# Optimization experiments

Measured on AMD Instinct MI355X. Metric: run time of the kernel, lower is better.

## Reference

```python
import jax, jax.numpy as jnp
import numpy as np

N = 30000        # nodes
E = 480000       # edges (before self-loops)
F_IN = 512       # input feature dim
HID = 64         # per-head hidden dim
HEADS = 4
WIDTH = HID * HEADS  # 256, concat heads
LAYERS = 3
NCLS = 40
NEG_SLOPE = 0.2


def setup_inputs() -> dict:
    key = jax.random.key(0)
    ks = jax.random.split(key, 16)
    def p(k, shape, scale=0.1):
        return jax.random.normal(k, shape, dtype=jnp.float32) * scale
    return {
        "x": jax.random.normal(ks[0], (N, F_IN), dtype=jnp.float32),
        "edge_index": jax.random.randint(ks[1], (2, E), 0, N, dtype=jnp.int32),
        # layer 1: F_IN -> HEADS*HID (concat)
        "W1": p(ks[2], (F_IN, WIDTH)), "as1": p(ks[3], (HEADS, HID)), "ad1": p(ks[4], (HEADS, HID)), "b1": p(ks[5], (WIDTH,)),
        # layer 2: WIDTH -> WIDTH
        "W2": p(ks[6], (WIDTH, WIDTH)), "as2": p(ks[7], (HEADS, HID)), "ad2": p(ks[8], (HEADS, HID)), "b2": p(ks[9], (WIDTH,)),
        # layer 3: WIDTH -> WIDTH
        "W3": p(ks[10], (WIDTH, WIDTH)), "as3": p(ks[11], (HEADS, HID)), "ad3": p(ks[12], (HEADS, HID)), "b3": p(ks[13], (WIDTH,)),
        # JK='cat' output head: WIDTH*LAYERS -> NCLS
        "Wo": p(ks[14], (WIDTH * LAYERS, NCLS)), "bo": p(ks[15], (NCLS,)),
    }


def gat_layer(x, Wm, a_src, a_dst, b, src, dst):
    # PyG GATConv (concat=True, eval mode): h = xW reshaped [N,H,C];
    # e_ij = leaky_relu(a_src.h_j + a_dst.h_i) for edge j->i, softmax over dst groups.
    n = x.shape[0]
    H, C = a_src.shape
    h = (x @ Wm).reshape(n, H, C)                      # [N,H,C]
    es = jnp.sum(h * a_src, axis=-1)                   # [N,H]
    ed = jnp.sum(h * a_dst, axis=-1)                   # [N,H]
    e = jax.nn.leaky_relu(es[src] + ed[dst], NEG_SLOPE)  # [Etot,H]
    m = jax.ops.segment_max(e, dst, num_segments=n)    # stable softmax per dst node
    w = jnp.exp(e - m[dst])
    den = jax.ops.segment_sum(w, dst, num_segments=n)
    alpha = w / den[dst]                               # [Etot,H]
    out = jax.ops.segment_sum(h[src] * alpha[:, :, None], dst, num_segments=n)  # [N,H,C]
    return out.reshape(n, H * C) + b


def reference(x, edge_index, W1, as1, ad1, b1, W2, as2, ad2, b2, W3, as3, ad3, b3, Wo, bo):
    # add self-loops (PyG GATConv default)
    loops = jnp.arange(N, dtype=edge_index.dtype)
    src = jnp.concatenate([edge_index[0], loops])
    dst = jnp.concatenate([edge_index[1], loops])
    # dropout is identity in eval mode
    h1 = jax.nn.relu(gat_layer(x, W1, as1, ad1, b1, src, dst))
    h2 = jax.nn.relu(gat_layer(h1, W2, as2, ad2, b2, src, dst))
    h3 = jax.nn.relu(gat_layer(h2, W3, as3, ad3, b3, src, dst))
    h = jnp.concatenate([h1, h2, h3], axis=-1)         # JK 'cat': [N, WIDTH*LAYERS]
    return h @ Wo + bo                                 # [N, NCLS]
```

## Files before the change

kernel.cpp:

```cpp
#include <hip/hip_runtime.h>

#define N_NODES 30000
#define N_EDGES 480000
#define ETOT    510000
#define F_IN    512
#define WIDTH   256
#define NCLS    40
#define KCAT    768
#define NPAD    48

typedef __attribute__((ext_vector_type(8))) short short8;
typedef __attribute__((ext_vector_type(4))) float f32x4;

__device__ __forceinline__ unsigned short f2bf(float f){
  unsigned u = __float_as_uint(f);
  u += 0x7fffu + ((u >> 16) & 1u);
  return (unsigned short)(u >> 16);
}
__device__ __forceinline__ float b2f(unsigned short s){
  return __uint_as_float(((unsigned)s) << 16);
}

__global__ void transpose_w_kernel(const float* __restrict__ W, unsigned short* __restrict__ Wt,
                                   int K, int Nc){
  int k = blockIdx.x * blockDim.x + threadIdx.x;
  int n = blockIdx.y;
  if (k < K) Wt[(size_t)n * K + k] = f2bf(W[(size_t)k * Nc + n]);
}

__global__ void transpose_wo_kernel(const float* __restrict__ Wo, unsigned short* __restrict__ WoT){
  int i = blockIdx.x * blockDim.x + threadIdx.x;
  if (i < NPAD * KCAT){
    int c = i / KCAT, k = i - c * KCAT;
    WoT[i] = (c < NCLS) ? f2bf(Wo[(size_t)k * NCLS + c]) : (unsigned short)0;
  }
}

__global__ void zero_kernel(int* __restrict__ p, int n){
  int i = blockIdx.x * blockDim.x + threadIdx.x;
  if (i < n) p[i] = 0;
}

__global__ void hist_kernel(const int* __restrict__ ei, int* __restrict__ counts){
  int e = blockIdx.x * blockDim.x + threadIdx.x;
  if (e < ETOT){
    int d = (e < N_EDGES) ? ei[N_EDGES + e] : (e - N_EDGES);
    atomicAdd(&counts[d], 1);
  }
}

__global__ __launch_bounds__(1024) void scan_kernel(const int* __restrict__ counts,
                                                    int* __restrict__ offsets,
                                                    int* __restrict__ cursor, int n){
  __shared__ int wsum[16];
  int tid = threadIdx.x, lane = tid & 63, wid = tid >> 6;
  int running = 0;
  int nchunks = (n + 1023) >> 10;
  for (int ch = 0; ch < nchunks; ++ch){
    int i = (ch << 10) + tid;
    int v = (i < n) ? counts[i] : 0;
    int x = v;
    #pragma unroll
    for (int off = 1; off < 64; off <<= 1){
      int t = __shfl_up(x, off, 64);
      if (lane >= off) x += t;
    }
    if (lane == 63) wsum[wid] = x;
    __syncthreads();
    if (wid == 0){
      int s = (lane < 16) ? wsum[lane] : 0;
      #pragma unroll
      for (int off = 1; off < 16; off <<= 1){
        int t = __shfl_up(s, off, 64);
        if (lane >= off) s += t;
      }
      if (lane < 16) wsum[lane] = s;
    }
    __syncthreads();
    int waveprefix = (wid > 0) ? wsum[wid - 1] : 0;
    int excl = x - v + waveprefix + running;
    if (i < n){ offsets[i] = excl; cursor[i] = excl; }
    running += wsum[15];
    __syncthreads();
  }
  if (tid == 0) offsets[n] = running;
}

__global__ void scatter_kernel(const int* __restrict__ ei, int* __restrict__ cursor,
                               int* __restrict__ srcs){
  int e = blockIdx.x * blockDim.x + threadIdx.x;
  if (e < ETOT){
    int s, d;
    if (e < N_EDGES){ s = ei[e]; d = ei[N_EDGES + e]; }
    else { s = e - N_EDGES; d = s; }
    int pos = atomicAdd(&cursor[d], 1);
    srcs[pos] = s;
  }
}

#define BM 64
#define BK 32

template<bool AF32>
__global__ __launch_bounds__(256) void gemm_fused_kernel(const void* __restrict__ Araw,
                                                         const unsigned short* __restrict__ Bt,
                                                         const float* __restrict__ a_s,
                                                         const float* __restrict__ a_d,
                                                         float* __restrict__ es,
                                                         float* __restrict__ ed,
                                                         unsigned short* __restrict__ hb,
                                                         int M, int K){
  __shared__ unsigned short Als[4 * 64 * 8];
  __shared__ unsigned short Bls[4 * 256 * 8];
  int tid = threadIdx.x;
  int lane = tid & 63, wid = tid >> 6;
  int l15 = lane & 15, quad = lane >> 4;
  int m0 = blockIdx.x * BM;

  f32x4 acc[4][4];
  #pragma unroll
  for (int rt = 0; rt < 4; ++rt)
    #pragma unroll
    for (int ct = 0; ct < 4; ++ct) acc[rt][ct] = (f32x4){0.f, 0.f, 0.f, 0.f};

  int ar = tid & 63, ac = tid >> 6;
  int agrow = m0 + ar; if (agrow >= M) agrow = M - 1;

  for (int k0 = 0; k0 < K; k0 += BK){
    __syncthreads();
    if (AF32){
      const float* Af = (const float*)Araw + (size_t)agrow * K + k0 + 8 * ac;
      float4 v0 = *(const float4*)(Af);
      float4 v1 = *(const float4*)(Af + 4);
      ushort4 p0 = {f2bf(v0.x), f2bf(v0.y), f2bf(v0.z), f2bf(v0.w)};
      ushort4 p1 = {f2bf(v1.x), f2bf(v1.y), f2bf(v1.z), f2bf(v1.w)};
      *(ushort4*)(&Als[(ac * 64 + ar) * 8])     = p0;
      *(ushort4*)(&Als[(ac * 64 + ar) * 8 + 4]) = p1;
    } else {
      const unsigned short* Ab = (const unsigned short*)Araw;
      uint4 av = *(const uint4*)(Ab + (size_t)agrow * K + k0 + 8 * ac);
      *(uint4*)(&Als[(ac * 64 + ar) * 8]) = av;
    }
    {
      const unsigned short* src = Bt + (size_t)tid * K + k0;
      uint4 b0 = *(const uint4*)(src);
      uint4 b1 = *(const uint4*)(src + 8);
      uint4 b2 = *(const uint4*)(src + 16);
      uint4 b3 = *(const uint4*)(src + 24);
      *(uint4*)(&Bls[(0 * 256 + tid) * 8]) = b0;
      *(uint4*)(&Bls[(1 * 256 + tid) * 8]) = b1;
      *(uint4*)(&Bls[(2 * 256 + tid) * 8]) = b2;
      *(uint4*)(&Bls[(3 * 256 + tid) * 8]) = b3;
    }
    __syncthreads();
    short8 af[4], bf[4];
    #pragma unroll
    for (int rt = 0; rt < 4; ++rt)
      af[rt] = *(const short8*)(&Als[(quad * 64 + rt * 16 + l15) * 8]);
    #pragma unroll
    for (int ct = 0; ct < 4; ++ct)
      bf[ct] = *(const short8*)(&Bls[(quad * 256 + wid * 64 + ct * 16 + l15) * 8]);
    #pragma unroll
    for (int rt = 0; rt < 4; ++rt)
      #pragma unroll
      for (int ct = 0; ct < 4; ++ct)
        acc[rt][ct] = __builtin_amdgcn_mfma_f32_16x16x32_bf16(af[rt], bf[ct], acc[rt][ct], 0, 0, 0);
  }

  int colbase = wid * 64;

  #pragma unroll
  for (int rt = 0; rt < 4; ++rt){
    int row0 = m0 + rt * 16 + quad * 4;
    #pragma unroll
    for (int i = 0; i < 4; ++i){
      int grow = row0 + i;
      unsigned vo[4];
      #pragma unroll
      for (int ct = 0; ct < 4; ++ct){
        unsigned lo = (unsigned)f2bf(acc[rt][ct][i]);
        unsigned hi = (unsigned)__shfl_xor((int)lo, 1, 64);
        vo[ct] = lo | (hi << 16);
      }
      if ((l15 & 1) == 0 && grow < M){
        unsigned short* hrow = hb + (size_t)grow * WIDTH + colbase + l15;
        *(unsigned*)(hrow)      = vo[0];
        *(unsigned*)(hrow + 16) = vo[1];
        *(unsigned*)(hrow + 32) = vo[2];
        *(unsigned*)(hrow + 48) = vo[3];
      }
    }
  }

  float asv[4], adv[4];
  #pragma unroll
  for (int ct = 0; ct < 4; ++ct){
    asv[ct] = a_s[wid * 64 + ct * 16 + l15];
    adv[ct] = a_d[wid * 64 + ct * 16 + l15];
  }
  #pragma unroll
  for (int rt = 0; rt < 4; ++rt){
    int row0 = m0 + rt * 16 + quad * 4;
    #pragma unroll
    for (int i = 0; i < 4; ++i){
      float se = acc[rt][0][i] * asv[0] + acc[rt][1][i] * asv[1]
               + acc[rt][2][i] * asv[2] + acc[rt][3][i] * asv[3];
      float sd = acc[rt][0][i] * adv[0] + acc[rt][1][i] * adv[1]
               + acc[rt][2][i] * adv[2] + acc[rt][3][i] * adv[3];
      #pragma unroll
      for (int off = 1; off < 16; off <<= 1){
        se += __shfl_xor(se, off, 64);
        sd += __shfl_xor(sd, off, 64);
      }
      int grow = row0 + i;
      if (l15 == 0 && grow < M){
        es[grow * 4 + wid] = se;
        ed[grow * 4 + wid] = sd;
      }
    }
  }
}

__global__ __launch_bounds__(256) void agg_kernel(const int* __restrict__ offsets,
                                                  const int* __restrict__ srcs,
                                                  const float* __restrict__ es,
                                                  const float* __restrict__ ed,
                                                  const unsigned short* __restrict__ hb,
                                                  const float* __restrict__ bias,
                                                  unsigned short* __restrict__ hout){
  __shared__ float eLds[8][64][4];
  __shared__ int   sLds[8][64];
  int wid = threadIdx.x >> 6;
  int lane = threadIdx.x & 63;
  int half = lane >> 5, l32 = lane & 31;
  int slot = wid * 2 + half;
  int n = blockIdx.x * 8 + slot;
  int base = offsets[n];
  int deg = offsets[n + 1] - base;
  float4 edv = *(const float4*)(ed + n * 4);

  float m0 = -1e30f, m1 = -1e30f, m2 = -1e30f, m3 = -1e30f;
  for (int i = l32; i < deg; i += 32){
    int s = srcs[base + i];
    float4 ev = *(const float4*)(es + s * 4);
    float e0 = ev.x + edv.x, e1 = ev.y + edv.y, e2 = ev.z + edv.z, e3 = ev.w + edv.w;
    e0 = e0 > 0.f ? e0 : 0.2f * e0;
    e1 = e1 > 0.f ? e1 : 0.2f * e1;
    e2 = e2 > 0.f ? e2 : 0.2f * e2;
    e3 = e3 > 0.f ? e3 : 0.2f * e3;
    if (i < 64){
      sLds[slot][i] = s;
      *(float4*)(&eLds[slot][i][0]) = (float4){e0, e1, e2, e3};
    }
    m0 = fmaxf(m0, e0); m1 = fmaxf(m1, e1); m2 = fmaxf(m2, e2); m3 = fmaxf(m3, e3);
  }
  #pragma unroll
  for (int off = 1; off < 32; off <<= 1){
    m0 = fmaxf(m0, __shfl_xor(m0, off, 64));
    m1 = fmaxf(m1, __shfl_xor(m1, off, 64));
    m2 = fmaxf(m2, __shfl_xor(m2, off, 64));
    m3 = fmaxf(m3, __shfl_xor(m3, off, 64));
  }
  int head = l32 >> 3;
  float mh  = (head == 0) ? m0 : (head == 1) ? m1 : (head == 2) ? m2 : m3;
  float edh = (head == 0) ? edv.x : (head == 1) ? edv.y : (head == 2) ? edv.z : edv.w;

  float2 a0 = {0.f,0.f}, a1 = {0.f,0.f}, a2 = {0.f,0.f}, a3 = {0.f,0.f};
  float den = 0.f;
  const unsigned short* hcol = hb + 8 * l32;
  for (int i = 0; i < deg; i += 8){
    int sidx[8]; float w[8];
    #pragma unroll
    for (int u = 0; u < 8; ++u){
      int idx = i + u;
      bool v = idx < deg;
      float le; int s;
      if (idx < 64 || !v){
        int ic = v ? idx : 0;
        if (ic >= 64) ic = 0;
        s  = sLds[slot][ic];
        le = eLds[slot][ic][head];
      } else {
        s = srcs[base + idx];
        float e = es[s * 4 + head] + edh;
        le = e > 0.f ? e : 0.2f * e;
      }
      sidx[u] = s;
      w[u] = v ? __expf(le - mh) : 0.f;
    }
    uint4 hv[8];
    #pragma unroll
    for (int u = 0; u < 8; ++u)
      hv[u] = *(const uint4*)(hcol + (size_t)sidx[u] * WIDTH);
    #pragma unroll
    for (int u = 0; u < 8; ++u){
      float wu = w[u];
      den += wu;
      a0.x += wu * __uint_as_float(hv[u].x << 16);
      a0.y += wu * __uint_as_float(hv[u].x & 0xffff0000u);
      a1.x += wu * __uint_as_float(hv[u].y << 16);
      a1.y += wu * __uint_as_float(hv[u].y & 0xffff0000u);
      a2.x += wu * __uint_as_float(hv[u].z << 16);
      a2.y += wu * __uint_as_float(hv[u].z & 0xffff0000u);
      a3.x += wu * __uint_as_float(hv[u].w << 16);
      a3.y += wu * __uint_as_float(hv[u].w & 0xffff0000u);
    }
  }
  float inv = 1.0f / den;
  const float* bp = bias + 8 * l32;
  float4 bv0 = *(const float4*)(bp);
  float4 bv1 = *(const float4*)(bp + 4);
  float o0 = fmaxf(a0.x * inv + bv0.x, 0.f);
  float o1 = fmaxf(a0.y * inv + bv0.y, 0.f);
  float o2 = fmaxf(a1.x * inv + bv0.z, 0.f);
  float o3 = fmaxf(a1.y * inv + bv0.w, 0.f);
  float o4 = fmaxf(a2.x * inv + bv1.x, 0.f);
  float o5 = fmaxf(a2.y * inv + bv1.y, 0.f);
  float o6 = fmaxf(a3.x * inv + bv1.z, 0.f);
  float o7 = fmaxf(a3.y * inv + bv1.w, 0.f);
  uint4 o;
  o.x = (unsigned)f2bf(o0) | ((unsigned)f2bf(o1) << 16);
  o.y = (unsigned)f2bf(o2) | ((unsigned)f2bf(o3) << 16);
  o.z = (unsigned)f2bf(o4) | ((unsigned)f2bf(o5) << 16);
  o.w = (unsigned)f2bf(o6) | ((unsigned)f2bf(o7) << 16);
  *(uint4*)(hout + (size_t)n * WIDTH + 8 * l32) = o;
}

__global__ __launch_bounds__(256) void out_gemm_kernel(const unsigned short* __restrict__ h1,
                                                       const unsigned short* __restrict__ h2,
                                                       const unsigned short* __restrict__ h3,
                                                       const unsigned short* __restrict__ WoT,
                                                       const float* __restrict__ bo,
                                                       float* __restrict__ out){
  int tid = threadIdx.x, lane = tid & 63, wid = tid >> 6;
  int l15 = lane & 15, quad = lane >> 4;
  int m0 = blockIdx.x * 64 + 16 * wid;

  f32x4 acc[3];
  #pragma unroll
  for (int t = 0; t < 3; ++t) acc[t] = (f32x4){0.f, 0.f, 0.f, 0.f};

  int arow = m0 + l15; if (arow >= N_NODES) arow = N_NODES - 1;

  #pragma unroll
  for (int part = 0; part < 3; ++part){
    const unsigned short* hp = (part == 0) ? h1 : (part == 1) ? h2 : h3;
    const unsigned short* ap = hp + (size_t)arow * WIDTH;
    #pragma unroll
    for (int k0 = 0; k0 < WIDTH; k0 += 32){
      short8 af = *(const short8*)(ap + k0 + quad * 8);
      int kk = part * WIDTH + k0;
      #pragma unroll
      for (int t = 0; t < 3; ++t){
        short8 bf = *(const short8*)(WoT + (size_t)(16 * t + l15) * KCAT + kk + quad * 8);
        acc[t] = __builtin_amdgcn_mfma_f32_16x16x32_bf16(af, bf, acc[t], 0, 0, 0);
      }
    }
  }

  int r0 = m0 + quad * 4;
  #pragma unroll
  for (int t = 0; t < 3; ++t){
    int col = 16 * t + l15;
    if (col < NCLS){
      float bc = bo[col];
      #pragma unroll
      for (int r = 0; r < 4; ++r){
        int grow = r0 + r;
        if (grow < N_NODES) out[(size_t)grow * NCLS + col] = acc[t][r] + bc;
      }
    }
  }
}

static inline size_t align256(size_t x){ return (x + 255) & ~(size_t)255; }

extern "C" void kernel_launch(void* const* d_in, const int* in_sizes, int n_in,
                              void* d_out, int out_size, void* d_ws, size_t ws_size,
                              hipStream_t stream) {
  const float* x   = (const float*)d_in[0];
  const int*   ei  = (const int*)  d_in[1];
  const float* W1  = (const float*)d_in[2];
  const float* as1 = (const float*)d_in[3];
  const float* ad1 = (const float*)d_in[4];
  const float* b1  = (const float*)d_in[5];
  const float* W2  = (const float*)d_in[6];
  const float* as2 = (const float*)d_in[7];
  const float* ad2 = (const float*)d_in[8];
  const float* b2  = (const float*)d_in[9];
  const float* W3  = (const float*)d_in[10];
  const float* as3 = (const float*)d_in[11];
  const float* ad3 = (const float*)d_in[12];
  const float* b3  = (const float*)d_in[13];
  const float* Wo  = (const float*)d_in[14];
  const float* bo  = (const float*)d_in[15];
  float* out = (float*)d_out;

  char* p = (char*)d_ws;
  auto take = [&](size_t bytes) -> char* { char* cur = p; p += align256(bytes); return cur; };

  unsigned short* Wt1   = (unsigned short*)take((size_t)WIDTH * F_IN * 2);
  unsigned short* Wt2   = (unsigned short*)take((size_t)WIDTH * WIDTH * 2);
  unsigned short* Wt3   = (unsigned short*)take((size_t)WIDTH * WIDTH * 2);
  unsigned short* WoT   = (unsigned short*)take((size_t)NPAD * KCAT * 2);
  unsigned short* hstage= (unsigned short*)take((size_t)N_NODES * WIDTH * 2);
  float*          es    = (float*)take((size_t)N_NODES * 4 * 4);
  float*          ed    = (float*)take((size_t)N_NODES * 4 * 4);
  unsigned short* h1b   = (unsigned short*)take((size_t)N_NODES * WIDTH * 2);
  unsigned short* h2b   = (unsigned short*)take((size_t)N_NODES * WIDTH * 2);
  unsigned short* h3b   = (unsigned short*)take((size_t)N_NODES * WIDTH * 2);
  int*            counts  = (int*)take((size_t)N_NODES * 4);
  int*            offsets = (int*)take((size_t)(N_NODES + 1) * 4);
  int*            cursor  = (int*)take((size_t)N_NODES * 4);
  int*            srcs    = (int*)take((size_t)ETOT * 4);

  transpose_w_kernel<<<dim3(F_IN / 256, WIDTH), 256, 0, stream>>>(W1, Wt1, F_IN, WIDTH);
  transpose_w_kernel<<<dim3(1, WIDTH), 256, 0, stream>>>(W2, Wt2, WIDTH, WIDTH);
  transpose_w_kernel<<<dim3(1, WIDTH), 256, 0, stream>>>(W3, Wt3, WIDTH, WIDTH);
  transpose_wo_kernel<<<(NPAD * KCAT + 255) / 256, 256, 0, stream>>>(Wo, WoT);

  zero_kernel<<<(N_NODES + 255) / 256, 256, 0, stream>>>(counts, N_NODES);
  hist_kernel<<<(ETOT + 255) / 256, 256, 0, stream>>>(ei, counts);
  scan_kernel<<<1, 1024, 0, stream>>>(counts, offsets, cursor, N_NODES);
  scatter_kernel<<<(ETOT + 255) / 256, 256, 0, stream>>>(ei, cursor, srcs);

  const int gemm_grid = (N_NODES + BM - 1) / BM;
  const int agg_grid  = N_NODES / 8;

  gemm_fused_kernel<true><<<gemm_grid, 256, 0, stream>>>(x, Wt1, as1, ad1, es, ed, hstage, N_NODES, F_IN);
  agg_kernel<<<agg_grid, 256, 0, stream>>>(offsets, srcs, es, ed, hstage, b1, h1b);
  gemm_fused_kernel<false><<<gemm_grid, 256, 0, stream>>>(h1b, Wt2, as2, ad2, es, ed, hstage, N_NODES, WIDTH);
  agg_kernel<<<agg_grid, 256, 0, stream>>>(offsets, srcs, es, ed, hstage, b2, h2b);
  gemm_fused_kernel<false><<<gemm_grid, 256, 0, stream>>>(h2b, Wt3, as3, ad3, es, ed, hstage, N_NODES, WIDTH);
  agg_kernel<<<agg_grid, 256, 0, stream>>>(offsets, srcs, es, ed, hstage, b3, h3b);

  out_gemm_kernel<<<gemm_grid, 256, 0, stream>>>(h1b, h2b, h3b, WoT, bo, out);
}
```

Baseline: 417.2 us.

## Halve GEMM row tile and prefetch next K-slice into registers

The fused projection GEMM now uses 32-row tiles instead of 64, doubling the grid to about 938 blocks for better CU occupancy. Global loads for the next K step are issued into registers before the current step's MFMAs, so memory latency overlaps with compute. The output GEMM keeps its 64-row grid through a separate grid constant. In exchange, each block re-reads the full weight matrix for half as many rows, doubling weight traffic, and the prefetch registers add pressure.

```diff
diff --git a/kernel.cpp b/kernel.cpp
--- a/kernel.cpp
+++ b/kernel.cpp
@@ -98,7 +98,7 @@
   }
 }
 
-#define BM 64
+#define BM 32
 #define BK 32
 
 template<bool AF32>
@@ -110,58 +110,70 @@
                                                          float* __restrict__ ed,
                                                          unsigned short* __restrict__ hb,
                                                          int M, int K){
-  __shared__ unsigned short Als[4 * 64 * 8];
+  __shared__ unsigned short Als[4 * 32 * 8];
   __shared__ unsigned short Bls[4 * 256 * 8];
   int tid = threadIdx.x;
   int lane = tid & 63, wid = tid >> 6;
   int l15 = lane & 15, quad = lane >> 4;
   int m0 = blockIdx.x * BM;
 
-  f32x4 acc[4][4];
-  #pragma unroll
-  for (int rt = 0; rt < 4; ++rt)
+  f32x4 acc[2][4];
+  #pragma unroll
+  for (int rt = 0; rt < 2; ++rt)
     #pragma unroll
     for (int ct = 0; ct < 4; ++ct) acc[rt][ct] = (f32x4){0.f, 0.f, 0.f, 0.f};
 
-  int ar = tid & 63, ac = tid >> 6;
+  int ar = tid & 31, ac = (tid >> 5) & 3;
+  bool a_active = tid < 128;
   int agrow = m0 + ar; if (agrow >= M) agrow = M - 1;
-
+  const float*          Afbase = (const float*)Araw + (size_t)agrow * K + 8 * ac;
+  const unsigned short* Abbase = (const unsigned short*)Araw + (size_t)agrow * K + 8 * ac;
+  const unsigned short* Bbase  = Bt + (size_t)tid * K;
+
+  uint4 pb0, pb1, pb2, pb3, pa;
+
+  auto load_step = [&](int k0){
+    const unsigned short* src = Bbase + k0;
+    pb0 = *(const uint4*)(src);
+    pb1 = *(const uint4*)(src + 8);
+    pb2 = *(const uint4*)(src + 16);
+    pb3 = *(const uint4*)(src + 24);
+    if (a_active){
+      if (AF32){
+        float4 v0 = *(const float4*)(Afbase + k0);
+        float4 v1 = *(const float4*)(Afbase + k0 + 4);
+        pa.x = (unsigned)f2bf(v0.x) | ((unsigned)f2bf(v0.y) << 16);
+        pa.y = (unsigned)f2bf(v0.z) | ((unsigned)f2bf(v0.w) << 16);
+        pa.z = (unsigned)f2bf(v1.x) | ((unsigned)f2bf(v1.y) << 16);
+        pa.w = (unsigned)f2bf(v1.z) | ((unsigned)f2bf(v1.w) << 16);
+      } else {
+        pa = *(const uint4*)(Abbase + k0);
+      }
+    }
+  };
+  auto store_step = [&](){
+    *(uint4*)(&Bls[(0 * 256 + tid) * 8]) = pb0;
+    *(uint4*)(&Bls[(1 * 256 + tid) * 8]) = pb1;
+    *(uint4*)(&Bls[(2 * 256 + tid) * 8]) = pb2;
+    *(uint4*)(&Bls[(3 * 256 + tid) * 8]) = pb3;
+    if (a_active) *(uint4*)(&Als[(ac * 32 + ar) * 8]) = pa;
+  };
+
+  load_step(0);
   for (int k0 = 0; k0 < K; k0 += BK){
     __syncthreads();
-    if (AF32){
-      const float* Af = (const float*)Araw + (size_t)agrow * K + k0 + 8 * ac;
-      float4 v0 = *(const float4*)(Af);
-      float4 v1 = *(const float4*)(Af + 4);
-      ushort4 p0 = {f2bf(v0.x), f2bf(v0.y), f2bf(v0.z), f2bf(v0.w)};
-      ushort4 p1 = {f2bf(v1.x), f2bf(v1.y), f2bf(v1.z), f2bf(v1.w)};
-      *(ushort4*)(&Als[(ac * 64 + ar) * 8])     = p0;
-      *(ushort4*)(&Als[(ac * 64 + ar) * 8 + 4]) = p1;
-    } else {
-      const unsigned short* Ab = (const unsigned short*)Araw;
-      uint4 av = *(const uint4*)(Ab + (size_t)agrow * K + k0 + 8 * ac);
-      *(uint4*)(&Als[(ac * 64 + ar) * 8]) = av;
-    }
-    {
-      const unsigned short* src = Bt + (size_t)tid * K + k0;
-      uint4 b0 = *(const uint4*)(src);
-      uint4 b1 = *(const uint4*)(src + 8);
-      uint4 b2 = *(const uint4*)(src + 16);
-      uint4 b3 = *(const uint4*)(src + 24);
-      *(uint4*)(&Bls[(0 * 256 + tid) * 8]) = b0;
-      *(uint4*)(&Bls[(1 * 256 + tid) * 8]) = b1;
-      *(uint4*)(&Bls[(2 * 256 + tid) * 8]) = b2;
-      *(uint4*)(&Bls[(3 * 256 + tid) * 8]) = b3;
-    }
+    store_step();
     __syncthreads();
-    short8 af[4], bf[4];
-    #pragma unroll
-    for (int rt = 0; rt < 4; ++rt)
-      af[rt] = *(const short8*)(&Als[(quad * 64 + rt * 16 + l15) * 8]);
+    if (k0 + BK < K) load_step(k0 + BK);
+    short8 af[2], bf[4];
+    #pragma unroll
+    for (int rt = 0; rt < 2; ++rt)
+      af[rt] = *(const short8*)(&Als[(quad * 32 + rt * 16 + l15) * 8]);
     #pragma unroll
     for (int ct = 0; ct < 4; ++ct)
       bf[ct] = *(const short8*)(&Bls[(quad * 256 + wid * 64 + ct * 16 + l15) * 8]);
     #pragma unroll
-    for (int rt = 0; rt < 4; ++rt)
+    for (int rt = 0; rt < 2; ++rt)
       #pragma unroll
       for (int ct = 0; ct < 4; ++ct)
         acc[rt][ct] = __builtin_amdgcn_mfma_f32_16x16x32_bf16(af[rt], bf[ct], acc[rt][ct], 0, 0, 0);
@@ -170,7 +182,7 @@
   int colbase = wid * 64;
 
   #pragma unroll
-  for (int rt = 0; rt < 4; ++rt){
+  for (int rt = 0; rt < 2; ++rt){
     int row0 = m0 + rt * 16 + quad * 4;
     #pragma unroll
     for (int i = 0; i < 4; ++i){
@@ -199,7 +211,7 @@
     adv[ct] = a_d[wid * 64 + ct * 16 + l15];
   }
   #pragma unroll
-  for (int rt = 0; rt < 4; ++rt){
+  for (int rt = 0; rt < 2; ++rt){
     int row0 = m0 + rt * 16 + quad * 4;
     #pragma unroll
     for (int i = 0; i < 4; ++i){
@@ -425,6 +437,7 @@
   scatter_kernel<<<(ETOT + 255) / 256, 256, 0, stream>>>(ei, cursor, srcs);
 
   const int gemm_grid = (N_NODES + BM - 1) / BM;
+  const int out_grid  = (N_NODES + 63) / 64;
   const int agg_grid  = N_NODES / 8;
 
   gemm_fused_kernel<true><<<gemm_grid, 256, 0, stream>>>(x, Wt1, as1, ad1, es, ed, hstage, N_NODES, F_IN);
@@ -434,5 +447,5 @@
   gemm_fused_kernel<false><<<gemm_grid, 256, 0, stream>>>(h2b, Wt3, as3, ad3, es, ed, hstage, N_NODES, WIDTH);
   agg_kernel<<<agg_grid, 256, 0, stream>>>(offsets, srcs, es, ed, hstage, b3, h3b);
 
-  out_gemm_kernel<<<gemm_grid, 256, 0, stream>>>(h1b, h2b, h3b, WoT, bo, out);
-}
+  out_gemm_kernel<<<out_grid, 256, 0, stream>>>(h1b, h2b, h3b, WoT, bo, out);
+}
```

After: 434.7 us. 1.04x slower.

## Restructure node GEMM: full-K weight slice resident in LDS, A fragments direct from global

Applied to the files above, without the earlier changes.

Each block now loads a 64-column slice of the transposed weight for the whole K dimension into shared memory once. Each wave then computes its own 64-row tile, reading A fragments straight from global memory into registers, with the next k-step prefetched. This removes the per-k-step shared-memory staging and the two block barriers per iteration. In exchange, A rows are re-read by the four column-group blocks, and each block holds a large LDS buffer (64 KB for K=512), which may limit occupancy.

```diff
diff --git a/kernel.cpp b/kernel.cpp
--- a/kernel.cpp
+++ b/kernel.cpp
@@ -98,24 +98,43 @@
   }
 }
 
-#define BM 64
-#define BK 32
-
-template<bool AF32>
-__global__ __launch_bounds__(256) void gemm_fused_kernel(const void* __restrict__ Araw,
-                                                         const unsigned short* __restrict__ Bt,
-                                                         const float* __restrict__ a_s,
-                                                         const float* __restrict__ a_d,
-                                                         float* __restrict__ es,
-                                                         float* __restrict__ ed,
-                                                         unsigned short* __restrict__ hb,
-                                                         int M, int K){
-  __shared__ unsigned short Als[4 * 64 * 8];
-  __shared__ unsigned short Bls[4 * 256 * 8];
-  int tid = threadIdx.x;
-  int lane = tid & 63, wid = tid >> 6;
+template<int K, bool AF32>
+__global__ __launch_bounds__(256) void gemm_persist_kernel(const void* __restrict__ Araw,
+                                                           const unsigned short* __restrict__ Bt,
+                                                           const float* __restrict__ a_s,
+                                                           const float* __restrict__ a_d,
+                                                           float* __restrict__ es,
+                                                           float* __restrict__ ed,
+                                                           unsigned short* __restrict__ hb,
+                                                           int M){
+  __shared__ unsigned short Bls[64 * K];
+  int tid = threadIdx.x, lane = tid & 63, wid = tid >> 6;
   int l15 = lane & 15, quad = lane >> 4;
-  int m0 = blockIdx.x * BM;
+  int g = blockIdx.x & 3;
+  int rblk = blockIdx.x >> 2;
+
+  {
+    int col = tid & 63, kc0 = tid >> 6;
+    const unsigned short* bsrc = Bt + (size_t)(64 * g + col) * K;
+    #pragma unroll
+    for (int kc = kc0; kc < K / 8; kc += 4){
+      uint4 v = *(const uint4*)(bsrc + kc * 8);
+      *(uint4*)(&Bls[(kc * 64 + col) * 8]) = v;
+    }
+  }
+  __syncthreads();
+
+  int tile = rblk * 4 + wid;
+  int ntiles = (M + 63) >> 6;
+  if (tile >= ntiles) return;
+  int m0 = tile * 64;
+
+  int arow[4];
+  #pragma unroll
+  for (int rt = 0; rt < 4; ++rt){
+    int r = m0 + rt * 16 + l15;
+    arow[rt] = (r < M) ? r : (M - 1);
+  }
 
   f32x4 acc[4][4];
   #pragma unroll
@@ -123,51 +142,42 @@
     #pragma unroll
     for (int ct = 0; ct < 4; ++ct) acc[rt][ct] = (f32x4){0.f, 0.f, 0.f, 0.f};
 
-  int ar = tid & 63, ac = tid >> 6;
-  int agrow = m0 + ar; if (agrow >= M) agrow = M - 1;
-
-  for (int k0 = 0; k0 < K; k0 += BK){
-    __syncthreads();
+  auto load_afrag = [&](int rt, int k0) -> short8 {
     if (AF32){
-      const float* Af = (const float*)Araw + (size_t)agrow * K + k0 + 8 * ac;
-      float4 v0 = *(const float4*)(Af);
-      float4 v1 = *(const float4*)(Af + 4);
-      ushort4 p0 = {f2bf(v0.x), f2bf(v0.y), f2bf(v0.z), f2bf(v0.w)};
-      ushort4 p1 = {f2bf(v1.x), f2bf(v1.y), f2bf(v1.z), f2bf(v1.w)};
-      *(ushort4*)(&Als[(ac * 64 + ar) * 8])     = p0;
-      *(ushort4*)(&Als[(ac * 64 + ar) * 8 + 4]) = p1;
+      const float* p = (const float*)Araw + (size_t)arow[rt] * K + k0 + quad * 8;
+      float4 v0 = *(const float4*)(p);
+      float4 v1 = *(const float4*)(p + 4);
+      union { short8 s; ushort4 u[2]; } r;
+      r.u[0] = (ushort4){f2bf(v0.x), f2bf(v0.y), f2bf(v0.z), f2bf(v0.w)};
+      r.u[1] = (ushort4){f2bf(v1.x), f2bf(v1.y), f2bf(v1.z), f2bf(v1.w)};
+      return r.s;
     } else {
-      const unsigned short* Ab = (const unsigned short*)Araw;
-      uint4 av = *(const uint4*)(Ab + (size_t)agrow * K + k0 + 8 * ac);
-      *(uint4*)(&Als[(ac * 64 + ar) * 8]) = av;
-    }
-    {
-      const unsigned short* src = Bt + (size_t)tid * K + k0;
-      uint4 b0 = *(const uint4*)(src);
-      uint4 b1 = *(const uint4*)(src + 8);
-      uint4 b2 = *(const uint4*)(src + 16);
-      uint4 b3 = *(const uint4*)(src + 24);
-      *(uint4*)(&Bls[(0 * 256 + tid) * 8]) = b0;
-      *(uint4*)(&Bls[(1 * 256 + tid) * 8]) = b1;
-      *(uint4*)(&Bls[(2 * 256 + tid) * 8]) = b2;
-      *(uint4*)(&Bls[(3 * 256 + tid) * 8]) = b3;
-    }
-    __syncthreads();
-    short8 af[4], bf[4];
+      return *(const short8*)((const unsigned short*)Araw + (size_t)arow[rt] * K + k0 + quad * 8);
+    }
+  };
+
+  short8 a_cur[4];
+  #pragma unroll
+  for (int rt = 0; rt < 4; ++rt) a_cur[rt] = load_afrag(rt, 0);
+
+  for (int k0 = 0; k0 < K; k0 += 32){
+    short8 a_nxt[4];
+    if (k0 + 32 < K){
+      #pragma unroll
+      for (int rt = 0; rt < 4; ++rt) a_nxt[rt] = load_afrag(rt, k0 + 32);
+    }
+    short8 bf[4];
+    #pragma unroll
+    for (int ct = 0; ct < 4; ++ct)
+      bf[ct] = *(const short8*)(&Bls[((k0 / 8 + quad) * 64 + ct * 16 + l15) * 8]);
     #pragma unroll
     for (int rt = 0; rt < 4; ++rt)
-      af[rt] = *(const short8*)(&Als[(quad * 64 + rt * 16 + l15) * 8]);
-    #pragma unroll
-    for (int ct = 0; ct < 4; ++ct)
-      bf[ct] = *(const short8*)(&Bls[(quad * 256 + wid * 64 + ct * 16 + l15) * 8]);
-    #pragma unroll
-    for (int rt = 0; rt < 4; ++rt)
       #pragma unroll
       for (int ct = 0; ct < 4; ++ct)
-        acc[rt][ct] = __builtin_amdgcn_mfma_f32_16x16x32_bf16(af[rt], bf[ct], acc[rt][ct], 0, 0, 0);
-  }
-
-  int colbase = wid * 64;
+        acc[rt][ct] = __builtin_amdgcn_mfma_f32_16x16x32_bf16(a_cur[rt], bf[ct], acc[rt][ct], 0, 0, 0);
+    #pragma unroll
+    for (int rt = 0; rt < 4; ++rt) a_cur[rt] = a_nxt[rt];
+  }
 
   #pragma unroll
   for (int rt = 0; rt < 4; ++rt){
@@ -183,7 +193,7 @@
         vo[ct] = lo | (hi << 16);
       }
       if ((l15 & 1) == 0 && grow < M){
-        unsigned short* hrow = hb + (size_t)grow * WIDTH + colbase + l15;
+        unsigned short* hrow = hb + (size_t)grow * WIDTH + 64 * g + l15;
         *(unsigned*)(hrow)      = vo[0];
         *(unsigned*)(hrow + 16) = vo[1];
         *(unsigned*)(hrow + 32) = vo[2];
@@ -195,8 +205,8 @@
   float asv[4], adv[4];
   #pragma unroll
   for (int ct = 0; ct < 4; ++ct){
-    asv[ct] = a_s[wid * 64 + ct * 16 + l15];
-    adv[ct] = a_d[wid * 64 + ct * 16 + l15];
+    asv[ct] = a_s[g * 64 + ct * 16 + l15];
+    adv[ct] = a_d[g * 64 + ct * 16 + l15];
   }
   #pragma unroll
   for (int rt = 0; rt < 4; ++rt){
@@ -214,8 +224,8 @@
       }
       int grow = row0 + i;
       if (l15 == 0 && grow < M){
-        es[grow * 4 + wid] = se;
-        ed[grow * 4 + wid] = sd;
+        es[grow * 4 + g] = se;
+        ed[grow * 4 + g] = sd;
       }
     }
   }
@@ -424,15 +434,17 @@
   scan_kernel<<<1, 1024, 0, stream>>>(counts, offsets, cursor, N_NODES);
   scatter_kernel<<<(ETOT + 255) / 256, 256, 0, stream>>>(ei, cursor, srcs);
 
-  const int gemm_grid = (N_NODES + BM - 1) / BM;
+  const int ntiles    = (N_NODES + 63) / 64;
+  const int gemm_grid = 4 * ((ntiles + 3) / 4);
+  const int out_grid  = ntiles;
   const int agg_grid  = N_NODES / 8;
 
-  gemm_fused_kernel<true><<<gemm_grid, 256, 0, stream>>>(x, Wt1, as1, ad1, es, ed, hstage, N_NODES, F_IN);
+  gemm_persist_kernel<F_IN, true><<<gemm_grid, 256, 0, stream>>>(x, Wt1, as1, ad1, es, ed, hstage, N_NODES);
   agg_kernel<<<agg_grid, 256, 0, stream>>>(offsets, srcs, es, ed, hstage, b1, h1b);
-  gemm_fused_kernel<false><<<gemm_grid, 256, 0, stream>>>(h1b, Wt2, as2, ad2, es, ed, hstage, N_NODES, WIDTH);
+  gemm_persist_kernel<WIDTH, false><<<gemm_grid, 256, 0, stream>>>(h1b, Wt2, as2, ad2, es, ed, hstage, N_NODES);
   agg_kernel<<<agg_grid, 256, 0, stream>>>(offsets, srcs, es, ed, hstage, b2, h2b);
-  gemm_fused_kernel<false><<<gemm_grid, 256, 0, stream>>>(h2b, Wt3, as3, ad3, es, ed, hstage, N_NODES, WIDTH);
+  gemm_persist_kernel<WIDTH, false><<<gemm_grid, 256, 0, stream>>>(h2b, Wt3, as3, ad3, es, ed, hstage, N_NODES);
   agg_kernel<<<agg_grid, 256, 0, stream>>>(offsets, srcs, es, ed, hstage, b3, h3b);
 
-  out_gemm_kernel<<<gemm_grid, 256, 0, stream>>>(h1b, h2b, h3b, WoT, bo, out);
-}
+  out_gemm_kernel<<<out_grid, 256, 0, stream>>>(h1b, h2b, h3b, WoT, bo, out);
+}
```

Result: no change. 417.4 us (+0.0%).
